# Kernel optimization log

Measured on AMD Instinct MI355X. Metric: run time of the kernel, lower is better.

Reference implementation:

```python
import jax, jax.numpy as jnp
import numpy as np

B, T, D, U = 64, 4096, 256, 64

def setup_inputs() -> dict:
    key = jax.random.key(0)
    k1, k2, k3 = jax.random.split(key, 3)
    inputs = jax.random.normal(k1, (B, T, D), dtype=jnp.float32)
    # glorot_uniform init for W (D,U) and u (U,1); zeros bias
    limW = float(np.sqrt(6.0 / (D + U)))
    W = jax.random.uniform(k2, (D, U), minval=-limW, maxval=limW, dtype=jnp.float32)
    limu = float(np.sqrt(6.0 / (U + 1)))
    u = jax.random.uniform(k3, (U, 1), minval=-limu, maxval=limu, dtype=jnp.float32)
    b = jnp.zeros((U,), dtype=jnp.float32)
    return {"inputs": inputs, "W": W, "b": b, "u": u}

def reference(inputs, W, b, u):
    # score: [B,T,U] = tanh(inputs @ W + b)
    score = jnp.tanh(jnp.einsum('btd,du->btu', inputs, W) + b)
    # logits: [B,T,1]; softmax over time axis (axis=1)
    logits = jnp.einsum('btu,uo->bto', score, u)
    attention_weights = jax.nn.softmax(logits, axis=1)
    # weighted sum over time -> [B,D]
    context = jnp.sum(inputs * attention_weights, axis=1)
    return (context, attention_weights)
```

## Files before the change

### kernel.cpp

```cpp
#include <hip/hip_runtime.h>
#include <math.h>

#define B_ 64
#define T_ 4096
#define D_ 256
#define U_ 64
#define TM 128
#define XSTRIDE 264

typedef float f32x4 __attribute__((ext_vector_type(4)));
typedef short bf16x8 __attribute__((ext_vector_type(8)));

__device__ __forceinline__ unsigned short f2bf_rne(float f) {
    unsigned u = __float_as_uint(f);
    unsigned r = u + 0x7fffu + ((u >> 16) & 1u);
    return (unsigned short)(r >> 16);
}
__device__ __forceinline__ float bfbits2f(unsigned short s) {
    return __uint_as_float(((unsigned)s) << 16);
}

__global__ __launch_bounds__(256) void wprep_kernel(
    const float* __restrict__ W, unsigned short* __restrict__ whi,
    unsigned short* __restrict__ wlo)
{
    int fi = blockIdx.x * 256 + threadIdx.x;
    int j    = fi & 7;
    int lane = (fi >> 3) & 63;
    int tile = fi >> 9;
    int nt = tile & 3, ks = tile >> 2;
    int k = ks * 32 + (lane >> 4) * 8 + j;
    int n = nt * 16 + (lane & 15);
    float w = W[k * U_ + n];
    unsigned short hi = f2bf_rne(w);
    unsigned short lo = f2bf_rne(w - bfbits2f(hi));
    whi[fi] = hi;
    wlo[fi] = lo;
}

__global__ __launch_bounds__(256) void fused_main(
    const float* __restrict__ x, const unsigned short* __restrict__ whi,
    const unsigned short* __restrict__ wlo, const float* __restrict__ bias,
    const float* __restrict__ uvec, float* __restrict__ wts,
    float* __restrict__ Zp, float* __restrict__ accZ)
{
    __shared__ unsigned short Xh[TM * XSTRIDE];
    __shared__ float esh[TM];
    __shared__ float red[8 * 256];
    __shared__ float zred[4];

    int tid = threadIdx.x;
    int lane = tid & 63, wid = tid >> 6;
    int q = lane >> 4, r = lane & 15;

    size_t R0 = (size_t)blockIdx.x * TM;
    int lrow0 = wid * 16 + r;
    int lrow1 = lrow0 + 64;
    const float* x0 = x + (R0 + lrow0) * D_;
    const float* x1 = x + (R0 + lrow1) * D_;

    f32x4 acc0[4], acc1[4];
#pragma unroll
    for (int nt = 0; nt < 4; ++nt) {
        acc0[nt] = (f32x4){0.f, 0.f, 0.f, 0.f};
        acc1[nt] = (f32x4){0.f, 0.f, 0.f, 0.f};
    }

    const bf16x8* BhV = (const bf16x8*)whi;
    const bf16x8* BlV = (const bf16x8*)wlo;

#pragma unroll 4
    for (int ks = 0; ks < 8; ++ks) {
        int k0 = ks * 32 + q * 8;
        float4 va0 = *(const float4*)(x0 + k0);
        float4 vb0 = *(const float4*)(x0 + k0 + 4);
        float4 va1 = *(const float4*)(x1 + k0);
        float4 vb1 = *(const float4*)(x1 + k0 + 4);
        float f0[8] = {va0.x, va0.y, va0.z, va0.w, vb0.x, vb0.y, vb0.z, vb0.w};
        float f1[8] = {va1.x, va1.y, va1.z, va1.w, vb1.x, vb1.y, vb1.z, vb1.w};
        union { bf16x8 v; unsigned short s[8]; uint4 u; } h0, l0, h1, l1;
#pragma unroll
        for (int j = 0; j < 8; ++j) {
            unsigned short a = f2bf_rne(f0[j]);
            h0.s[j] = a;
            l0.s[j] = f2bf_rne(f0[j] - bfbits2f(a));
            unsigned short c = f2bf_rne(f1[j]);
            h1.s[j] = c;
            l1.s[j] = f2bf_rne(f1[j] - bfbits2f(c));
        }
        *(uint4*)(&Xh[lrow0 * XSTRIDE + k0]) = h0.u;
        *(uint4*)(&Xh[lrow1 * XSTRIDE + k0]) = h1.u;
#pragma unroll
        for (int nt = 0; nt < 4; ++nt) {
            bf16x8 bh = BhV[(ks * 4 + nt) * 64 + lane];
            bf16x8 bl = BlV[(ks * 4 + nt) * 64 + lane];
            acc0[nt] = __builtin_amdgcn_mfma_f32_16x16x32_bf16(h0.v, bh, acc0[nt], 0, 0, 0);
            acc0[nt] = __builtin_amdgcn_mfma_f32_16x16x32_bf16(h0.v, bl, acc0[nt], 0, 0, 0);
            acc0[nt] = __builtin_amdgcn_mfma_f32_16x16x32_bf16(l0.v, bh, acc0[nt], 0, 0, 0);
            acc1[nt] = __builtin_amdgcn_mfma_f32_16x16x32_bf16(h1.v, bh, acc1[nt], 0, 0, 0);
            acc1[nt] = __builtin_amdgcn_mfma_f32_16x16x32_bf16(h1.v, bl, acc1[nt], 0, 0, 0);
            acc1[nt] = __builtin_amdgcn_mfma_f32_16x16x32_bf16(l1.v, bh, acc1[nt], 0, 0, 0);
        }
    }

    float zsum = 0.f;
#pragma unroll
    for (int s = 0; s < 2; ++s) {
        f32x4* A = s ? acc1 : acc0;
        float p0 = 0.f, p1 = 0.f, p2 = 0.f, p3 = 0.f;
#pragma unroll
        for (int nt = 0; nt < 4; ++nt) {
            int col = nt * 16 + r;
            float bv = bias[col], uv = uvec[col];
            float s0 = A[nt][0] + bv, s1 = A[nt][1] + bv,
                  s2 = A[nt][2] + bv, s3 = A[nt][3] + bv;
            p0 = fmaf(1.f - 2.f / (__expf(2.f * s0) + 1.f), uv, p0);
            p1 = fmaf(1.f - 2.f / (__expf(2.f * s1) + 1.f), uv, p1);
            p2 = fmaf(1.f - 2.f / (__expf(2.f * s2) + 1.f), uv, p2);
            p3 = fmaf(1.f - 2.f / (__expf(2.f * s3) + 1.f), uv, p3);
        }
#pragma unroll
        for (int off = 1; off < 16; off <<= 1) {
            p0 += __shfl_xor(p0, off, 64);
            p1 += __shfl_xor(p1, off, 64);
            p2 += __shfl_xor(p2, off, 64);
            p3 += __shfl_xor(p3, off, 64);
        }
        float e0 = __expf(p0), e1 = __expf(p1), e2 = __expf(p2), e3 = __expf(p3);
        if (r == 0) {
            float4 o = {e0, e1, e2, e3};
            int lr = s * 64 + wid * 16 + q * 4;
            *(float4*)(wts + R0 + lr) = o;
            *(float4*)(&esh[lr]) = o;
        }
        zsum += (e0 + e1) + (e2 + e3);
    }
    zsum += __shfl_xor(zsum, 16, 64);
    zsum += __shfl_xor(zsum, 32, 64);
    if (lane == 0) zred[wid] = zsum;
    __syncthreads();
    if (tid == 0) Zp[blockIdx.x] = (zred[0] + zred[1]) + (zred[2] + zred[3]);

    int colg = tid & 31, ph = tid >> 5;
    float pacc[8];
#pragma unroll
    for (int j = 0; j < 8; ++j) pacc[j] = 0.f;
#pragma unroll 4
    for (int i = 0; i < TM; i += 8) {
        int row = i + ph;
        float w = esh[row];
        union { uint4 u; unsigned short s[8]; } v;
        v.u = *(const uint4*)(&Xh[row * XSTRIDE + colg * 8]);
#pragma unroll
        for (int j = 0; j < 8; ++j)
            pacc[j] = fmaf(w, bfbits2f(v.s[j]), pacc[j]);
    }
    float4* redv = (float4*)(&red[ph * 256 + colg * 8]);
    redv[0] = (float4){pacc[0], pacc[1], pacc[2], pacc[3]};
    redv[1] = (float4){pacc[4], pacc[5], pacc[6], pacc[7]};
    __syncthreads();
    float ssum = 0.f;
#pragma unroll
    for (int p = 0; p < 8; ++p) ssum += red[p * 256 + tid];
    int b = blockIdx.x >> 5;
    atomicAdd(&accZ[b * D_ + tid], ssum);
}

__global__ __launch_bounds__(256) void finalize_kernel(
    float* __restrict__ wts, const float* __restrict__ Zp,
    const float* __restrict__ accZ, float* __restrict__ ctx)
{
    int b = blockIdx.x;
    int tid = threadIdx.x;
    float Z = 0.f;
#pragma unroll
    for (int i = 0; i < T_ / TM; ++i) Z += Zp[b * (T_ / TM) + i];
    float invZ = 1.f / Z;

    ctx[b * D_ + tid] = accZ[b * D_ + tid] * invZ;

    float4* wp = (float4*)(wts + (size_t)b * T_);
#pragma unroll
    for (int i = 0; i < T_ / 4 / 256; ++i) {
        float4 v = wp[tid + i * 256];
        v.x *= invZ; v.y *= invZ; v.z *= invZ; v.w *= invZ;
        wp[tid + i * 256] = v;
    }
}

extern "C" void kernel_launch(void* const* d_in, const int* in_sizes, int n_in,
                              void* d_out, int out_size, void* d_ws, size_t ws_size,
                              hipStream_t stream) {
    const float* x    = (const float*)d_in[0];
    const float* W    = (const float*)d_in[1];
    const float* bias = (const float*)d_in[2];
    const float* uvec = (const float*)d_in[3];

    float* out = (float*)d_out;
    float* ctx = out;
    float* wts = out + B_ * D_;

    unsigned short* whi = (unsigned short*)d_ws;
    unsigned short* wlo = whi + D_ * U_;
    float* Zp   = (float*)(wlo + D_ * U_);
    float* accZ = Zp + (B_ * T_) / TM;

    hipMemsetAsync(accZ, 0, B_ * D_ * sizeof(float), stream);

    wprep_kernel<<<D_ * U_ / 256, 256, 0, stream>>>(W, whi, wlo);
    fused_main<<<(B_ * T_) / TM, 256, 0, stream>>>(x, whi, wlo, bias, uvec, wts, Zp, accZ);
    finalize_kernel<<<B_, 256, 0, stream>>>(wts, Zp, accZ, ctx);
}
```

Baseline: 435.9 us.

## Persistent chunked blocks with register double-buffered x and fp32 weighted sum

Each block now processes 512 rows in 64-row chunks instead of one 128-row tile, double-buffering x loads in registers so the next chunk's global reads overlap the current chunk's MFMA and tanh work. W hi/lo is staged into LDS once per block. The weighted context sum is accumulated in fp32 registers from the original x values rather than from a bf16 copy in LDS, then reduced across lanes and waves. This cuts grid size to 512 blocks and removes the per-tile LDS X store and atomic traffic. In exchange it carries heavy register pressure (64 accumulators plus 32 float4 buffers) and fewer blocks to hide latency.

After: 677.2 us. 55.4% more time.

```diff
diff --git a/kernel.cpp b/kernel.cpp
--- a/kernel.cpp
+++ b/kernel.cpp
@@ -5,8 +5,9 @@
 #define T_ 4096
 #define D_ 256
 #define U_ 64
-#define TM 128
-#define XSTRIDE 264
+#define CH 64
+#define NCHUNK 8
+#define BPB 8
 
 typedef float f32x4 __attribute__((ext_vector_type(4)));
 typedef short bf16x8 __attribute__((ext_vector_type(8)));
@@ -38,132 +39,162 @@
     wlo[fi] = lo;
 }
 
-__global__ __launch_bounds__(256) void fused_main(
+#define LOAD_CHUNK(c, xb)                                              \
+    do {                                                               \
+        const float* xp_ = xbase + (size_t)(c) * CH * D_;              \
+        _Pragma("unroll")                                              \
+        for (int ks_ = 0; ks_ < 8; ++ks_) {                            \
+            xb[2 * ks_]     = *(const float4*)(xp_ + ks_ * 32);        \
+            xb[2 * ks_ + 1] = *(const float4*)(xp_ + ks_ * 32 + 4);    \
+        }                                                              \
+    } while (0)
+
+#define COMPUTE_CHUNK(c, xb)                                                        \
+    do {                                                                            \
+        f32x4 acc[4];                                                               \
+        _Pragma("unroll")                                                           \
+        for (int nt_ = 0; nt_ < 4; ++nt_) acc[nt_] = (f32x4){0.f, 0.f, 0.f, 0.f};   \
+        _Pragma("unroll")                                                           \
+        for (int ks_ = 0; ks_ < 8; ++ks_) {                                         \
+            float4 va_ = xb[2 * ks_], vb_ = xb[2 * ks_ + 1];                        \
+            float f_[8] = {va_.x, va_.y, va_.z, va_.w, vb_.x, vb_.y, vb_.z, vb_.w}; \
+            union { bf16x8 v; unsigned short s[8]; } hi_, lo_;                      \
+            _Pragma("unroll")                                                       \
+            for (int j_ = 0; j_ < 8; ++j_) {                                        \
+                unsigned short a_ = f2bf_rne(f_[j_]);                               \
+                hi_.s[j_] = a_;                                                     \
+                lo_.s[j_] = f2bf_rne(f_[j_] - bfbits2f(a_));                        \
+            }                                                                       \
+            _Pragma("unroll")                                                       \
+            for (int nt_ = 0; nt_ < 4; ++nt_) {                                     \
+                bf16x8 bh_ = BhV[(ks_ * 4 + nt_) * 64 + lane];                      \
+                bf16x8 bl_ = BlV[(ks_ * 4 + nt_) * 64 + lane];                      \
+                acc[nt_] = __builtin_amdgcn_mfma_f32_16x16x32_bf16(hi_.v, bh_, acc[nt_], 0, 0, 0); \
+                acc[nt_] = __builtin_amdgcn_mfma_f32_16x16x32_bf16(hi_.v, bl_, acc[nt_], 0, 0, 0); \
+                acc[nt_] = __builtin_amdgcn_mfma_f32_16x16x32_bf16(lo_.v, bh_, acc[nt_], 0, 0, 0); \
+            }                                                                       \
+        }                                                                           \
+        float p0_ = 0.f, p1_ = 0.f, p2_ = 0.f, p3_ = 0.f;                           \
+        _Pragma("unroll")                                                           \
+        for (int nt_ = 0; nt_ < 4; ++nt_) {                                         \
+            int col_ = nt_ * 16 + r;                                                \
+            float bv_ = bias[col_], uv_ = uvec[col_];                               \
+            float s0_ = acc[nt_][0] + bv_, s1_ = acc[nt_][1] + bv_,                 \
+                  s2_ = acc[nt_][2] + bv_, s3_ = acc[nt_][3] + bv_;                 \
+            p0_ = fmaf(1.f - 2.f / (__expf(2.f * s0_) + 1.f), uv_, p0_);            \
+            p1_ = fmaf(1.f - 2.f / (__expf(2.f * s1_) + 1.f), uv_, p1_);            \
+            p2_ = fmaf(1.f - 2.f / (__expf(2.f * s2_) + 1.f), uv_, p2_);            \
+            p3_ = fmaf(1.f - 2.f / (__expf(2.f * s3_) + 1.f), uv_, p3_);            \
+        }                                                                           \
+        _Pragma("unroll")                                                           \
+        for (int off_ = 1; off_ < 16; off_ <<= 1) {                                 \
+            p0_ += __shfl_xor(p0_, off_, 64);                                       \
+            p1_ += __shfl_xor(p1_, off_, 64);                                       \
+            p2_ += __shfl_xor(p2_, off_, 64);                                       \
+            p3_ += __shfl_xor(p3_, off_, 64);                                       \
+        }                                                                           \
+        float e0_ = __expf(p0_), e1_ = __expf(p1_),                                 \
+              e2_ = __expf(p2_), e3_ = __expf(p3_);                                 \
+        if (r == 0) {                                                               \
+            float4 o_ = {e0_, e1_, e2_, e3_};                                       \
+            *(float4*)(wbase + (c) * CH + wid * 16 + q * 4) = o_;                   \
+        }                                                                           \
+        zacc += (e0_ + e1_) + (e2_ + e3_);                                          \
+        int src_ = (r >> 2) * 16;                                                   \
+        float ea_ = __shfl(e0_, src_, 64), eb_ = __shfl(e1_, src_, 64),             \
+              ec_ = __shfl(e2_, src_, 64), ed_ = __shfl(e3_, src_, 64);             \
+        float er_ = (r & 2) ? ((r & 1) ? ed_ : ec_) : ((r & 1) ? eb_ : ea_);        \
+        _Pragma("unroll")                                                           \
+        for (int ks_ = 0; ks_ < 8; ++ks_) {                                         \
+            float4 va_ = xb[2 * ks_], vb_ = xb[2 * ks_ + 1];                        \
+            P[ks_ * 8 + 0] = fmaf(er_, va_.x, P[ks_ * 8 + 0]);                      \
+            P[ks_ * 8 + 1] = fmaf(er_, va_.y, P[ks_ * 8 + 1]);                      \
+            P[ks_ * 8 + 2] = fmaf(er_, va_.z, P[ks_ * 8 + 2]);                      \
+            P[ks_ * 8 + 3] = fmaf(er_, va_.w, P[ks_ * 8 + 3]);                      \
+            P[ks_ * 8 + 4] = fmaf(er_, vb_.x, P[ks_ * 8 + 4]);                      \
+            P[ks_ * 8 + 5] = fmaf(er_, vb_.y, P[ks_ * 8 + 5]);                      \
+            P[ks_ * 8 + 6] = fmaf(er_, vb_.z, P[ks_ * 8 + 6]);                      \
+            P[ks_ * 8 + 7] = fmaf(er_, vb_.w, P[ks_ * 8 + 7]);                      \
+        }                                                                           \
+    } while (0)
+
+__global__ __launch_bounds__(256, 2) void fused_main(
     const float* __restrict__ x, const unsigned short* __restrict__ whi,
     const unsigned short* __restrict__ wlo, const float* __restrict__ bias,
     const float* __restrict__ uvec, float* __restrict__ wts,
     float* __restrict__ Zp, float* __restrict__ accZ)
 {
-    __shared__ unsigned short Xh[TM * XSTRIDE];
-    __shared__ float esh[TM];
-    __shared__ float red[8 * 256];
+    __shared__ unsigned short Bh[16384];
+    __shared__ unsigned short Bl[16384];
+    __shared__ float pred[16 * 64];
     __shared__ float zred[4];
 
     int tid = threadIdx.x;
+    {
+        const uint4* sh = (const uint4*)whi;
+        const uint4* sl = (const uint4*)wlo;
+        uint4* dh = (uint4*)Bh;
+        uint4* dl = (uint4*)Bl;
+#pragma unroll
+        for (int i = 0; i < 8; ++i) {
+            dh[tid + i * 256] = sh[tid + i * 256];
+            dl[tid + i * 256] = sl[tid + i * 256];
+        }
+    }
+    __syncthreads();
+
     int lane = tid & 63, wid = tid >> 6;
     int q = lane >> 4, r = lane & 15;
-
-    size_t R0 = (size_t)blockIdx.x * TM;
-    int lrow0 = wid * 16 + r;
-    int lrow1 = lrow0 + 64;
-    const float* x0 = x + (R0 + lrow0) * D_;
-    const float* x1 = x + (R0 + lrow1) * D_;
-
-    f32x4 acc0[4], acc1[4];
-#pragma unroll
-    for (int nt = 0; nt < 4; ++nt) {
-        acc0[nt] = (f32x4){0.f, 0.f, 0.f, 0.f};
-        acc1[nt] = (f32x4){0.f, 0.f, 0.f, 0.f};
-    }
-
-    const bf16x8* BhV = (const bf16x8*)whi;
-    const bf16x8* BlV = (const bf16x8*)wlo;
-
-#pragma unroll 4
-    for (int ks = 0; ks < 8; ++ks) {
-        int k0 = ks * 32 + q * 8;
-        float4 va0 = *(const float4*)(x0 + k0);
-        float4 vb0 = *(const float4*)(x0 + k0 + 4);
-        float4 va1 = *(const float4*)(x1 + k0);
-        float4 vb1 = *(const float4*)(x1 + k0 + 4);
-        float f0[8] = {va0.x, va0.y, va0.z, va0.w, vb0.x, vb0.y, vb0.z, vb0.w};
-        float f1[8] = {va1.x, va1.y, va1.z, va1.w, vb1.x, vb1.y, vb1.z, vb1.w};
-        union { bf16x8 v; unsigned short s[8]; uint4 u; } h0, l0, h1, l1;
-#pragma unroll
-        for (int j = 0; j < 8; ++j) {
-            unsigned short a = f2bf_rne(f0[j]);
-            h0.s[j] = a;
-            l0.s[j] = f2bf_rne(f0[j] - bfbits2f(a));
-            unsigned short c = f2bf_rne(f1[j]);
-            h1.s[j] = c;
-            l1.s[j] = f2bf_rne(f1[j] - bfbits2f(c));
-        }
-        *(uint4*)(&Xh[lrow0 * XSTRIDE + k0]) = h0.u;
-        *(uint4*)(&Xh[lrow1 * XSTRIDE + k0]) = h1.u;
-#pragma unroll
-        for (int nt = 0; nt < 4; ++nt) {
-            bf16x8 bh = BhV[(ks * 4 + nt) * 64 + lane];
-            bf16x8 bl = BlV[(ks * 4 + nt) * 64 + lane];
-            acc0[nt] = __builtin_amdgcn_mfma_f32_16x16x32_bf16(h0.v, bh, acc0[nt], 0, 0, 0);
-            acc0[nt] = __builtin_amdgcn_mfma_f32_16x16x32_bf16(h0.v, bl, acc0[nt], 0, 0, 0);
-            acc0[nt] = __builtin_amdgcn_mfma_f32_16x16x32_bf16(l0.v, bh, acc0[nt], 0, 0, 0);
-            acc1[nt] = __builtin_amdgcn_mfma_f32_16x16x32_bf16(h1.v, bh, acc1[nt], 0, 0, 0);
-            acc1[nt] = __builtin_amdgcn_mfma_f32_16x16x32_bf16(h1.v, bl, acc1[nt], 0, 0, 0);
-            acc1[nt] = __builtin_amdgcn_mfma_f32_16x16x32_bf16(l1.v, bh, acc1[nt], 0, 0, 0);
-        }
-    }
-
-    float zsum = 0.f;
-#pragma unroll
-    for (int s = 0; s < 2; ++s) {
-        f32x4* A = s ? acc1 : acc0;
-        float p0 = 0.f, p1 = 0.f, p2 = 0.f, p3 = 0.f;
-#pragma unroll
-        for (int nt = 0; nt < 4; ++nt) {
-            int col = nt * 16 + r;
-            float bv = bias[col], uv = uvec[col];
-            float s0 = A[nt][0] + bv, s1 = A[nt][1] + bv,
-                  s2 = A[nt][2] + bv, s3 = A[nt][3] + bv;
-            p0 = fmaf(1.f - 2.f / (__expf(2.f * s0) + 1.f), uv, p0);
-            p1 = fmaf(1.f - 2.f / (__expf(2.f * s1) + 1.f), uv, p1);
-            p2 = fmaf(1.f - 2.f / (__expf(2.f * s2) + 1.f), uv, p2);
-            p3 = fmaf(1.f - 2.f / (__expf(2.f * s3) + 1.f), uv, p3);
-        }
-#pragma unroll
-        for (int off = 1; off < 16; off <<= 1) {
-            p0 += __shfl_xor(p0, off, 64);
-            p1 += __shfl_xor(p1, off, 64);
-            p2 += __shfl_xor(p2, off, 64);
-            p3 += __shfl_xor(p3, off, 64);
-        }
-        float e0 = __expf(p0), e1 = __expf(p1), e2 = __expf(p2), e3 = __expf(p3);
-        if (r == 0) {
-            float4 o = {e0, e1, e2, e3};
-            int lr = s * 64 + wid * 16 + q * 4;
-            *(float4*)(wts + R0 + lr) = o;
-            *(float4*)(&esh[lr]) = o;
-        }
-        zsum += (e0 + e1) + (e2 + e3);
-    }
-    zsum += __shfl_xor(zsum, 16, 64);
-    zsum += __shfl_xor(zsum, 32, 64);
-    if (lane == 0) zred[wid] = zsum;
+    int b = blockIdx.x / BPB;
+    int pb = blockIdx.x % BPB;
+    size_t row00 = (size_t)b * T_ + (size_t)pb * (CH * NCHUNK);
+    const float* xbase = x + (row00 + wid * 16 + r) * D_ + q * 8;
+    float* wbase = wts + row00;
+
+    const bf16x8* BhV = (const bf16x8*)Bh;
+    const bf16x8* BlV = (const bf16x8*)Bl;
+
+    float P[64];
+#pragma unroll
+    for (int i = 0; i < 64; ++i) P[i] = 0.f;
+    float zacc = 0.f;
+
+    float4 xb0[16], xb1[16];
+
+    LOAD_CHUNK(0, xb0);
+    for (int c = 0; c < NCHUNK; c += 2) {
+        LOAD_CHUNK(c + 1, xb1);
+        COMPUTE_CHUNK(c, xb0);
+        if (c + 2 < NCHUNK) LOAD_CHUNK(c + 2, xb0);
+        COMPUTE_CHUNK(c + 1, xb1);
+    }
+
+#pragma unroll
+    for (int i = 0; i < 64; ++i) {
+        P[i] += __shfl_xor(P[i], 1, 64);
+        P[i] += __shfl_xor(P[i], 2, 64);
+        P[i] += __shfl_xor(P[i], 4, 64);
+        P[i] += __shfl_xor(P[i], 8, 64);
+    }
+    if (r == 0) {
+        float* pd = &pred[(wid * 4 + q) * 64];
+#pragma unroll
+        for (int i = 0; i < 16; ++i)
+            *(float4*)(pd + i * 4) =
+                (float4){P[4 * i], P[4 * i + 1], P[4 * i + 2], P[4 * i + 3]};
+    }
+    zacc += __shfl_xor(zacc, 16, 64);
+    zacc += __shfl_xor(zacc, 32, 64);
+    if (lane == 0) zred[wid] = zacc;
     __syncthreads();
     if (tid == 0) Zp[blockIdx.x] = (zred[0] + zred[1]) + (zred[2] + zred[3]);
 
-    int colg = tid & 31, ph = tid >> 5;
-    float pacc[8];
-#pragma unroll
-    for (int j = 0; j < 8; ++j) pacc[j] = 0.f;
-#pragma unroll 4
-    for (int i = 0; i < TM; i += 8) {
-        int row = i + ph;
-        float w = esh[row];
-        union { uint4 u; unsigned short s[8]; } v;
-        v.u = *(const uint4*)(&Xh[row * XSTRIDE + colg * 8]);
-#pragma unroll
-        for (int j = 0; j < 8; ++j)
-            pacc[j] = fmaf(w, bfbits2f(v.s[j]), pacc[j]);
-    }
-    float4* redv = (float4*)(&red[ph * 256 + colg * 8]);
-    redv[0] = (float4){pacc[0], pacc[1], pacc[2], pacc[3]};
-    redv[1] = (float4){pacc[4], pacc[5], pacc[6], pacc[7]};
-    __syncthreads();
-    float ssum = 0.f;
-#pragma unroll
-    for (int p = 0; p < 8; ++p) ssum += red[p * 256 + tid];
-    int b = blockIdx.x >> 5;
-    atomicAdd(&accZ[b * D_ + tid], ssum);
+    int d = tid;
+    int ksd = d >> 5, qd = (d >> 3) & 3, jd = d & 7;
+    int idx = ksd * 8 + jd;
+    float s = (pred[(0 * 4 + qd) * 64 + idx] + pred[(1 * 4 + qd) * 64 + idx]) +
+              (pred[(2 * 4 + qd) * 64 + idx] + pred[(3 * 4 + qd) * 64 + idx]);
+    atomicAdd(&accZ[b * D_ + d], s);
 }
 
 __global__ __launch_bounds__(256) void finalize_kernel(
@@ -174,7 +205,7 @@
     int tid = threadIdx.x;
     float Z = 0.f;
 #pragma unroll
-    for (int i = 0; i < T_ / TM; ++i) Z += Zp[b * (T_ / TM) + i];
+    for (int i = 0; i < BPB; ++i) Z += Zp[b * BPB + i];
     float invZ = 1.f / Z;
 
     ctx[b * D_ + tid] = accZ[b * D_ + tid] * invZ;
@@ -203,11 +234,11 @@
     unsigned short* whi = (unsigned short*)d_ws;
     unsigned short* wlo = whi + D_ * U_;
     float* Zp   = (float*)(wlo + D_ * U_);
-    float* accZ = Zp + (B_ * T_) / TM;
+    float* accZ = Zp + B_ * BPB;
 
     hipMemsetAsync(accZ, 0, B_ * D_ * sizeof(float), stream);
 
     wprep_kernel<<<D_ * U_ / 256, 256, 0, stream>>>(W, whi, wlo);
-    fused_main<<<(B_ * T_) / TM, 256, 0, stream>>>(x, whi, wlo, bias, uvec, wts, Zp, accZ);
+    fused_main<<<B_ * BPB, 256, 0, stream>>>(x, whi, wlo, bias, uvec, wts, Zp, accZ);
     finalize_kernel<<<B_, 256, 0, stream>>>(wts, Zp, accZ, ctx);
 }
```

## Stage W in LDS, loop row chunks per block, and replace atomics with partials

Applied to the files above, without the earlier changes.

Each block now handles 512 rows of one batch in 64-row chunks, with the bf16 hi/lo W splits copied once into shared memory. The weighted sum re-reads x from global memory in fp32 rather than keeping a bf16 copy in LDS. Per-block partial context vectors are written out and reduced in the finalize kernel, removing the memset and atomics. The cost is a second pass over x that relies on cache hits, and fewer rows in flight per wave.

Result: slower. 454.5 us (+4.3%).

```diff
diff --git a/kernel.cpp b/kernel.cpp
--- a/kernel.cpp
+++ b/kernel.cpp
@@ -5,8 +5,9 @@
 #define T_ 4096
 #define D_ 256
 #define U_ 64
-#define TM 128
-#define XSTRIDE 264
+#define BPB 8
+#define RPB (T_ / BPB)
+#define NCH (RPB / 64)
 
 typedef float f32x4 __attribute__((ext_vector_type(4)));
 typedef short bf16x8 __attribute__((ext_vector_type(8)));
@@ -38,82 +39,86 @@
     wlo[fi] = lo;
 }
 
-__global__ __launch_bounds__(256) void fused_main(
+__global__ __launch_bounds__(256, 2) void fused_main(
     const float* __restrict__ x, const unsigned short* __restrict__ whi,
     const unsigned short* __restrict__ wlo, const float* __restrict__ bias,
     const float* __restrict__ uvec, float* __restrict__ wts,
-    float* __restrict__ Zp, float* __restrict__ accZ)
+    float* __restrict__ Zp, float* __restrict__ Pp)
 {
-    __shared__ unsigned short Xh[TM * XSTRIDE];
-    __shared__ float esh[TM];
-    __shared__ float red[8 * 256];
+    __shared__ unsigned short Bh[16384];
+    __shared__ unsigned short Bl[16384];
+    __shared__ float esh[RPB];
     __shared__ float zred[4];
 
     int tid = threadIdx.x;
+    {
+        const uint4* sh = (const uint4*)whi;
+        const uint4* sl = (const uint4*)wlo;
+        uint4* dh = (uint4*)Bh;
+        uint4* dl = (uint4*)Bl;
+#pragma unroll
+        for (int i = 0; i < 8; ++i) {
+            dh[tid + i * 256] = sh[tid + i * 256];
+            dl[tid + i * 256] = sl[tid + i * 256];
+        }
+    }
+    __syncthreads();
+
     int lane = tid & 63, wid = tid >> 6;
     int q = lane >> 4, r = lane & 15;
-
-    size_t R0 = (size_t)blockIdx.x * TM;
-    int lrow0 = wid * 16 + r;
-    int lrow1 = lrow0 + 64;
-    const float* x0 = x + (R0 + lrow0) * D_;
-    const float* x1 = x + (R0 + lrow1) * D_;
-
-    f32x4 acc0[4], acc1[4];
-#pragma unroll
-    for (int nt = 0; nt < 4; ++nt) {
-        acc0[nt] = (f32x4){0.f, 0.f, 0.f, 0.f};
-        acc1[nt] = (f32x4){0.f, 0.f, 0.f, 0.f};
-    }
-
-    const bf16x8* BhV = (const bf16x8*)whi;
-    const bf16x8* BlV = (const bf16x8*)wlo;
-
-#pragma unroll 4
-    for (int ks = 0; ks < 8; ++ks) {
-        int k0 = ks * 32 + q * 8;
-        float4 va0 = *(const float4*)(x0 + k0);
-        float4 vb0 = *(const float4*)(x0 + k0 + 4);
-        float4 va1 = *(const float4*)(x1 + k0);
-        float4 vb1 = *(const float4*)(x1 + k0 + 4);
-        float f0[8] = {va0.x, va0.y, va0.z, va0.w, vb0.x, vb0.y, vb0.z, vb0.w};
-        float f1[8] = {va1.x, va1.y, va1.z, va1.w, vb1.x, vb1.y, vb1.z, vb1.w};
-        union { bf16x8 v; unsigned short s[8]; uint4 u; } h0, l0, h1, l1;
-#pragma unroll
-        for (int j = 0; j < 8; ++j) {
-            unsigned short a = f2bf_rne(f0[j]);
-            h0.s[j] = a;
-            l0.s[j] = f2bf_rne(f0[j] - bfbits2f(a));
-            unsigned short c = f2bf_rne(f1[j]);
-            h1.s[j] = c;
-            l1.s[j] = f2bf_rne(f1[j] - bfbits2f(c));
-        }
-        *(uint4*)(&Xh[lrow0 * XSTRIDE + k0]) = h0.u;
-        *(uint4*)(&Xh[lrow1 * XSTRIDE + k0]) = h1.u;
-#pragma unroll
-        for (int nt = 0; nt < 4; ++nt) {
-            bf16x8 bh = BhV[(ks * 4 + nt) * 64 + lane];
-            bf16x8 bl = BlV[(ks * 4 + nt) * 64 + lane];
-            acc0[nt] = __builtin_amdgcn_mfma_f32_16x16x32_bf16(h0.v, bh, acc0[nt], 0, 0, 0);
-            acc0[nt] = __builtin_amdgcn_mfma_f32_16x16x32_bf16(h0.v, bl, acc0[nt], 0, 0, 0);
-            acc0[nt] = __builtin_amdgcn_mfma_f32_16x16x32_bf16(l0.v, bh, acc0[nt], 0, 0, 0);
-            acc1[nt] = __builtin_amdgcn_mfma_f32_16x16x32_bf16(h1.v, bh, acc1[nt], 0, 0, 0);
-            acc1[nt] = __builtin_amdgcn_mfma_f32_16x16x32_bf16(h1.v, bl, acc1[nt], 0, 0, 0);
-            acc1[nt] = __builtin_amdgcn_mfma_f32_16x16x32_bf16(l1.v, bh, acc1[nt], 0, 0, 0);
-        }
-    }
-
-    float zsum = 0.f;
-#pragma unroll
-    for (int s = 0; s < 2; ++s) {
-        f32x4* A = s ? acc1 : acc0;
+    int b = blockIdx.x / BPB;
+    int pb = blockIdx.x % BPB;
+    size_t row00 = (size_t)b * T_ + (size_t)pb * RPB;
+    const float* xlane = x + (row00 + wid * 16 + r) * D_ + q * 8;
+    float* wbase = wts + row00;
+
+    const bf16x8* BhV = (const bf16x8*)Bh;
+    const bf16x8* BlV = (const bf16x8*)Bl;
+
+    float zacc = 0.f;
+
+#pragma unroll 1
+    for (int c = 0; c < NCH; ++c) {
+        const float* xp = xlane + (size_t)c * 64 * D_;
+        float4 xb[16];
+#pragma unroll
+        for (int ks = 0; ks < 8; ++ks) {
+            xb[2 * ks]     = *(const float4*)(xp + ks * 32);
+            xb[2 * ks + 1] = *(const float4*)(xp + ks * 32 + 4);
+        }
+
+        f32x4 acc[4];
+#pragma unroll
+        for (int nt = 0; nt < 4; ++nt) acc[nt] = (f32x4){0.f, 0.f, 0.f, 0.f};
+
+#pragma unroll
+        for (int ks = 0; ks < 8; ++ks) {
+            float4 va = xb[2 * ks], vb = xb[2 * ks + 1];
+            float f[8] = {va.x, va.y, va.z, va.w, vb.x, vb.y, vb.z, vb.w};
+            union { bf16x8 v; unsigned short s[8]; } hi_, lo_;
+#pragma unroll
+            for (int j = 0; j < 8; ++j) {
+                unsigned short a = f2bf_rne(f[j]);
+                hi_.s[j] = a;
+                lo_.s[j] = f2bf_rne(f[j] - bfbits2f(a));
+            }
+#pragma unroll
+            for (int nt = 0; nt < 4; ++nt) {
+                bf16x8 bh = BhV[(ks * 4 + nt) * 64 + lane];
+                bf16x8 bl = BlV[(ks * 4 + nt) * 64 + lane];
+                acc[nt] = __builtin_amdgcn_mfma_f32_16x16x32_bf16(hi_.v, bh, acc[nt], 0, 0, 0);
+                acc[nt] = __builtin_amdgcn_mfma_f32_16x16x32_bf16(hi_.v, bl, acc[nt], 0, 0, 0);
+                acc[nt] = __builtin_amdgcn_mfma_f32_16x16x32_bf16(lo_.v, bh, acc[nt], 0, 0, 0);
+            }
+        }
+
         float p0 = 0.f, p1 = 0.f, p2 = 0.f, p3 = 0.f;
 #pragma unroll
         for (int nt = 0; nt < 4; ++nt) {
             int col = nt * 16 + r;
             float bv = bias[col], uv = uvec[col];
-            float s0 = A[nt][0] + bv, s1 = A[nt][1] + bv,
-                  s2 = A[nt][2] + bv, s3 = A[nt][3] + bv;
+            float s0 = acc[nt][0] + bv, s1 = acc[nt][1] + bv,
+                  s2 = acc[nt][2] + bv, s3 = acc[nt][3] + bv;
             p0 = fmaf(1.f - 2.f / (__expf(2.f * s0) + 1.f), uv, p0);
             p1 = fmaf(1.f - 2.f / (__expf(2.f * s1) + 1.f), uv, p1);
             p2 = fmaf(1.f - 2.f / (__expf(2.f * s2) + 1.f), uv, p2);
@@ -129,55 +134,56 @@
         float e0 = __expf(p0), e1 = __expf(p1), e2 = __expf(p2), e3 = __expf(p3);
         if (r == 0) {
             float4 o = {e0, e1, e2, e3};
-            int lr = s * 64 + wid * 16 + q * 4;
-            *(float4*)(wts + R0 + lr) = o;
+            int lr = c * 64 + wid * 16 + q * 4;
+            *(float4*)(wbase + lr) = o;
             *(float4*)(&esh[lr]) = o;
         }
-        zsum += (e0 + e1) + (e2 + e3);
-    }
-    zsum += __shfl_xor(zsum, 16, 64);
-    zsum += __shfl_xor(zsum, 32, 64);
-    if (lane == 0) zred[wid] = zsum;
+        zacc += (e0 + e1) + (e2 + e3);
+    }
+
+    zacc += __shfl_xor(zacc, 16, 64);
+    zacc += __shfl_xor(zacc, 32, 64);
+    if (lane == 0) zred[wid] = zacc;
     __syncthreads();
     if (tid == 0) Zp[blockIdx.x] = (zred[0] + zred[1]) + (zred[2] + zred[3]);
 
-    int colg = tid & 31, ph = tid >> 5;
-    float pacc[8];
-#pragma unroll
-    for (int j = 0; j < 8; ++j) pacc[j] = 0.f;
-#pragma unroll 4
-    for (int i = 0; i < TM; i += 8) {
-        int row = i + ph;
-        float w = esh[row];
-        union { uint4 u; unsigned short s[8]; } v;
-        v.u = *(const uint4*)(&Xh[row * XSTRIDE + colg * 8]);
-#pragma unroll
-        for (int j = 0; j < 8; ++j)
-            pacc[j] = fmaf(w, bfbits2f(v.s[j]), pacc[j]);
-    }
-    float4* redv = (float4*)(&red[ph * 256 + colg * 8]);
-    redv[0] = (float4){pacc[0], pacc[1], pacc[2], pacc[3]};
-    redv[1] = (float4){pacc[4], pacc[5], pacc[6], pacc[7]};
-    __syncthreads();
-    float ssum = 0.f;
-#pragma unroll
-    for (int p = 0; p < 8; ++p) ssum += red[p * 256 + tid];
-    int b = blockIdx.x >> 5;
-    atomicAdd(&accZ[b * D_ + tid], ssum);
+    const float* xc = x + row00 * D_ + tid;
+    float P0 = 0.f, P1 = 0.f, P2 = 0.f, P3 = 0.f;
+#pragma unroll 2
+    for (int row = 0; row < RPB; row += 8) {
+        float e0 = esh[row + 0], e1 = esh[row + 1], e2 = esh[row + 2], e3 = esh[row + 3];
+        float e4 = esh[row + 4], e5 = esh[row + 5], e6 = esh[row + 6], e7 = esh[row + 7];
+        float x0 = xc[(size_t)(row + 0) * D_];
+        float x1 = xc[(size_t)(row + 1) * D_];
+        float x2 = xc[(size_t)(row + 2) * D_];
+        float x3 = xc[(size_t)(row + 3) * D_];
+        float x4 = xc[(size_t)(row + 4) * D_];
+        float x5 = xc[(size_t)(row + 5) * D_];
+        float x6 = xc[(size_t)(row + 6) * D_];
+        float x7 = xc[(size_t)(row + 7) * D_];
+        P0 = fmaf(e0, x0, P0); P1 = fmaf(e1, x1, P1);
+        P2 = fmaf(e2, x2, P2); P3 = fmaf(e3, x3, P3);
+        P0 = fmaf(e4, x4, P0); P1 = fmaf(e5, x5, P1);
+        P2 = fmaf(e6, x6, P2); P3 = fmaf(e7, x7, P3);
+    }
+    Pp[(size_t)blockIdx.x * D_ + tid] = (P0 + P1) + (P2 + P3);
 }
 
 __global__ __launch_bounds__(256) void finalize_kernel(
     float* __restrict__ wts, const float* __restrict__ Zp,
-    const float* __restrict__ accZ, float* __restrict__ ctx)
+    const float* __restrict__ Pp, float* __restrict__ ctx)
 {
     int b = blockIdx.x;
     int tid = threadIdx.x;
     float Z = 0.f;
 #pragma unroll
-    for (int i = 0; i < T_ / TM; ++i) Z += Zp[b * (T_ / TM) + i];
+    for (int i = 0; i < BPB; ++i) Z += Zp[b * BPB + i];
     float invZ = 1.f / Z;
 
-    ctx[b * D_ + tid] = accZ[b * D_ + tid] * invZ;
+    float s = 0.f;
+#pragma unroll
+    for (int i = 0; i < BPB; ++i) s += Pp[(size_t)(b * BPB + i) * D_ + tid];
+    ctx[b * D_ + tid] = s * invZ;
 
     float4* wp = (float4*)(wts + (size_t)b * T_);
 #pragma unroll
@@ -202,12 +208,10 @@
 
     unsigned short* whi = (unsigned short*)d_ws;
     unsigned short* wlo = whi + D_ * U_;
-    float* Zp   = (float*)(wlo + D_ * U_);
-    float* accZ = Zp + (B_ * T_) / TM;
-
-    hipMemsetAsync(accZ, 0, B_ * D_ * sizeof(float), stream);
+    float* Zp = (float*)(wlo + D_ * U_);
+    float* Pp = Zp + B_ * BPB;
 
     wprep_kernel<<<D_ * U_ / 256, 256, 0, stream>>>(W, whi, wlo);
-    fused_main<<<(B_ * T_) / TM, 256, 0, stream>>>(x, whi, wlo, bias, uvec, wts, Zp, accZ);
-    finalize_kernel<<<B_, 256, 0, stream>>>(wts, Zp, accZ, ctx);
-}
+    fused_main<<<B_ * BPB, 256, 0, stream>>>(x, whi, wlo, bias, uvec, wts, Zp, Pp);
+    finalize_kernel<<<B_, 256, 0, stream>>>(wts, Zp, Pp, ctx);
+}
```
